# Performance work log

Hardware: AMD Instinct MI355X
Metric: run time of the kernel (lower is better)

Reference implementation:

```python
import jax, jax.numpy as jnp
import numpy as np

L = 16384   # nodes (rows)
E = 131072  # edges
SP = 20000  # column positions (nodes + periodic images)
C = 512     # embed_dim
H = 8       # heads
DH = C // H # head dim = 64
HID = 1024  # ffn hidden


def setup_inputs() -> dict:
    key = jax.random.key(0)
    ks = jax.random.split(key, 16)
    p = lambda k, shape: jax.random.normal(k, shape, dtype=jnp.float32) * 0.02
    return dict(
        x=jax.random.normal(ks[0], (L, C), dtype=jnp.float32),
        row_index=jax.random.randint(ks[1], (E,), 0, L),
        col_index=jax.random.randint(ks[2], (E,), 0, L),
        to_col_index=jax.random.randint(ks[3], (E,), 0, SP),
        att_bias=jax.random.normal(ks[4], (E, H), dtype=jnp.float32),
        pos_att_bias=jax.random.normal(ks[5], (E, H), dtype=jnp.float32),
        dist=jax.random.uniform(ks[6], (E,), minval=0.5, maxval=5.0),
        pos=jax.random.normal(ks[7], (L, 3), dtype=jnp.float32),
        col_pos=jax.random.normal(ks[8], (SP, 3), dtype=jnp.float32),
        ln1_g=jnp.ones((C,), jnp.float32), ln1_b=jnp.zeros((C,), jnp.float32),
        ln2_g=jnp.ones((C,), jnp.float32), ln2_b=jnp.zeros((C,), jnp.float32),
        Wq=p(ks[9], (C, C)), bq=jnp.zeros((C,), jnp.float32),
        Wk=p(ks[10], (C, C)), bk=jnp.zeros((C,), jnp.float32),
        Wv=p(ks[11], (C, C)), bv=jnp.zeros((C,), jnp.float32),
        Wvec=p(ks[12], (3, C)), bvec=jnp.zeros((C,), jnp.float32),
        Wo=p(ks[13], (C, C)), bo=jnp.zeros((C,), jnp.float32),
        W1=p(ks[14], (C, HID)), b1=jnp.zeros((HID,), jnp.float32),
        W2=p(ks[15], (HID, C)), b2=jnp.zeros((C,), jnp.float32),
    )


def _ln(x, g, b, eps=1e-5):
    mu = jnp.mean(x, -1, keepdims=True)
    v = jnp.mean((x - mu) ** 2, -1, keepdims=True)
    return (x - mu) * jax.lax.rsqrt(v + eps) * g + b


def reference(x, row_index, col_index, to_col_index, att_bias, pos_att_bias,
              dist, pos, col_pos, ln1_g, ln1_b, ln2_g, ln2_b,
              Wq, bq, Wk, bk, Wv, bv, Wvec, bvec, Wo, bo, W1, b1, W2, b2):
    Lx = x.shape[0]
    # --- pre-norm + Euclidean sparse attention ---
    z = _ln(x, ln1_g, ln1_b)
    q = (z @ Wq + bq).reshape(Lx, H, DH)
    k = (z @ Wk + bk).reshape(Lx, H, DH)
    v = (z @ Wv + bv).reshape(Lx, H, DH)
    qe = q[row_index]          # (E,H,DH) gather
    ke = k[col_index]          # (E,H,DH)
    ve = v[col_index]          # (E,H,DH)
    # relative unit direction from receiving node to (PBC-shifted) column node
    rel = (col_pos[to_col_index] - pos[row_index]) / dist[:, None]   # (E,3)
    ve = ve + (rel @ Wvec + bvec).reshape(-1, H, DH)
    # Euclidean (negative squared L2) attention score + positional bias
    score = -jnp.sum((qe - ke) ** 2, axis=-1) / np.float32(np.sqrt(DH)) + pos_att_bias  # (E,H)
    # segment softmax over edges grouped by row_index
    m = jax.ops.segment_max(score, row_index, num_segments=Lx)       # (L,H)
    m = jnp.where(jnp.isfinite(m), m, 0.0)
    pexp = jnp.exp(score - m[row_index])
    den = jax.ops.segment_sum(pexp, row_index, num_segments=Lx)      # (L,H)
    deng = den[row_index]
    alpha = pexp / jnp.where(deng == 0.0, 1.0, deng)                 # (E,H)
    out = jax.ops.segment_sum(alpha[:, :, None] * ve, row_index, num_segments=Lx)
    att = out.reshape(Lx, C) @ Wo + bo
    x = x + att
    # --- pre-norm + feed-forward ---
    z2 = _ln(x, ln2_g, ln2_b)
    ff = jax.nn.gelu(z2 @ W1 + b1) @ W2 + b2
    return x + ff
```

## Files before the change

### kernel.cpp

```cpp
#include <hip/hip_runtime.h>

#define L_NODES 16384
#define E_EDGES 131072
#define CDIM 512
#define QKVDIM 1536
#define HEADS 8
#define DHEAD 64
#define HID 1024

typedef __attribute__((ext_vector_type(8))) short bf16x8;
typedef __attribute__((ext_vector_type(4))) float f32x4;

__device__ inline unsigned short f2b(float f) {
    union { float f; unsigned int u; } v{f};
    unsigned int r = (v.u + 0x7fffu + ((v.u >> 16) & 1u)) >> 16;
    return (unsigned short)r;
}
__device__ inline float b2f(unsigned short h) {
    union { unsigned int u; float f; } v;
    v.u = (unsigned int)h << 16;
    return v.f;
}

__device__ inline void async_lds16(const void* g, void* l) {
    __builtin_amdgcn_global_load_lds(
        (const __attribute__((address_space(1))) unsigned int*)g,
        (__attribute__((address_space(3))) unsigned int*)l,
        16, 0, 0);
}

__global__ __launch_bounds__(256) void ln_bf16_kernel(
    const float* __restrict__ x, const float* __restrict__ g,
    const float* __restrict__ b, short* __restrict__ out)
{
    int row = blockIdx.x;
    int t = threadIdx.x;
    const float2* xr = (const float2*)(x + (size_t)row * CDIM);
    float2 v = xr[t];
    float s = v.x + v.y;
    float sq = v.x * v.x + v.y * v.y;
    for (int off = 32; off; off >>= 1) {
        s += __shfl_xor(s, off);
        sq += __shfl_xor(sq, off);
    }
    __shared__ float ss[4], sqs[4];
    int wave = t >> 6, lane = t & 63;
    if (lane == 0) { ss[wave] = s; sqs[wave] = sq; }
    __syncthreads();
    s = ss[0] + ss[1] + ss[2] + ss[3];
    sq = sqs[0] + sqs[1] + sqs[2] + sqs[3];
    float mu = s * (1.0f / CDIM);
    float var = sq * (1.0f / CDIM) - mu * mu;
    float inv = rsqrtf(var + 1e-5f);
    int c = t * 2;
    unsigned short h0 = f2b((v.x - mu) * inv * g[c] + b[c]);
    unsigned short h1 = f2b((v.y - mu) * inv * g[c + 1] + b[c + 1]);
    unsigned int packed = ((unsigned int)h1 << 16) | h0;
    *(unsigned int*)(out + (size_t)row * CDIM + c) = packed;
}

__global__ __launch_bounds__(256) void prep_kernel(
    const float* __restrict__ Wq, const float* __restrict__ Wk,
    const float* __restrict__ Wv, const float* __restrict__ Wo,
    const float* __restrict__ W1, const float* __restrict__ W2,
    short* __restrict__ wqkvT, short* __restrict__ woT,
    short* __restrict__ w1T, short* __restrict__ w2T,
    const float* __restrict__ bq, const float* __restrict__ bk,
    const float* __restrict__ bv, float* __restrict__ bqkv,
    int* __restrict__ cnt)
{
    int bid = blockIdx.x;
    if (bid >= 2054) {
        cnt[(bid - 2054) * 256 + threadIdx.x] = 0;
        return;
    }
    if (bid >= 2048) {
        int i = (bid - 2048) * 256 + threadIdx.x;
        float val = (i < CDIM) ? bq[i] : (i < 2 * CDIM) ? bk[i - CDIM] : bv[i - 2 * CDIM];
        bqkv[i] = val;
        return;
    }
    const float* W; short* WT; int K, N, tn, tk;
    if (bid < 1024) {
        int w = bid >> 8, local = bid & 255;
        tn = local & 15; tk = local >> 4; K = 512; N = 512;
        W = (w == 0) ? Wq : (w == 1) ? Wk : (w == 2) ? Wv : Wo;
        WT = (w == 3) ? woT : wqkvT + (size_t)w * 512 * 512;
    } else if (bid < 1536) {
        int local = bid - 1024;
        tn = local & 31; tk = local >> 5; K = 512; N = 1024;
        W = W1; WT = w1T;
    } else {
        int local = bid - 1536;
        tn = local & 15; tk = local >> 4; K = 1024; N = 512;
        W = W2; WT = w2T;
    }
    __shared__ float tile[32][33];
    int tx = threadIdx.x & 31, ty = threadIdx.x >> 5;
    int n0 = tn * 32, k0 = tk * 32;
#pragma unroll
    for (int r = 0; r < 4; r++)
        tile[ty + r * 8][tx] = W[(size_t)(k0 + ty + r * 8) * N + n0 + tx];
    __syncthreads();
#pragma unroll
    for (int r = 0; r < 4; r++)
        WT[(size_t)(n0 + ty + r * 8) * K + k0 + tx] = f2b(tile[tx][ty + r * 8]);
}

template<int BM>
__global__ __launch_bounds__(256) void gemm_bf16_kernel(
    const short* __restrict__ A, const short* __restrict__ B,
    const float* __restrict__ bias, const float* __restrict__ res,
    float* __restrict__ outf, short* __restrict__ outb,
    int M, int N, int K, int act)
{
    constexpr int MI = BM / 32;
    constexpr int LPI_A = BM / 64;
    constexpr int STAGE_A = BM * 64;
    constexpr int STAGE_B = 8192;
    __shared__ short As[3 * BM * 32];
    __shared__ short Bs[3 * 128 * 32];
    int t = threadIdx.x;
    int bm = blockIdx.y * BM, bn = blockIdx.x * 128;
    int wave = t >> 6, lane = t & 63;
    int wm = (wave & 1) * (BM / 2), wn = (wave >> 1) * 64;
    int crow = lane & 15, quad = lane >> 4;

    f32x4 acc[MI][4] = {};

    const int niter = K >> 5;
    auto stage = [&](int s, int k0) {
#pragma unroll
        for (int a = 0; a < LPI_A; a++) {
            int idx = a * 256 + t;
            int row = idx >> 2, chunk = idx & 3;
            async_lds16(A + (size_t)(bm + row) * K + k0 + chunk * 8,
                        (char*)As + s * STAGE_A + idx * 16);
        }
#pragma unroll
        for (int c = 0; c < 2; c++) {
            int idx = c * 256 + t;
            int row = idx >> 2, chunk = idx & 3;
            async_lds16(B + (size_t)(bn + row) * K + k0 + chunk * 8,
                        (char*)Bs + s * STAGE_B + idx * 16);
        }
    };

    stage(0, 0);
    stage(1, 32);

    for (int i = 0; i < niter; ++i) {
        int cur = i % 3;
        if (i + 1 < niter) {
            if constexpr (BM == 128) asm volatile("s_waitcnt vmcnt(4)" ::: "memory");
            else                     asm volatile("s_waitcnt vmcnt(3)" ::: "memory");
        } else {
            asm volatile("s_waitcnt vmcnt(0)" ::: "memory");
        }
        __builtin_amdgcn_s_barrier();
        if (i + 2 < niter) stage((i + 2) % 3, (i + 2) << 5);

        const short* Ab = As + cur * (BM * 32);
        const short* Bb = Bs + cur * (128 * 32);
        bf16x8 af[MI], bg[4];
#pragma unroll
        for (int ii = 0; ii < MI; ii++)
            af[ii] = *(const bf16x8*)&Ab[(wm + ii * 16 + crow) * 32 + quad * 8];
#pragma unroll
        for (int j = 0; j < 4; j++)
            bg[j] = *(const bf16x8*)&Bb[(wn + j * 16 + crow) * 32 + quad * 8];
#pragma unroll
        for (int ii = 0; ii < MI; ii++)
#pragma unroll
            for (int j = 0; j < 4; j++)
                acc[ii][j] = __builtin_amdgcn_mfma_f32_16x16x32_bf16(af[ii], bg[j], acc[ii][j], 0, 0, 0);
    }

#pragma unroll
    for (int i = 0; i < MI; i++) {
#pragma unroll
        for (int j = 0; j < 4; j++) {
            int n = bn + wn + j * 16 + crow;
            float bi = bias ? bias[n] : 0.0f;
#pragma unroll
            for (int r = 0; r < 4; r++) {
                int mrow = bm + wm + i * 16 + quad * 4 + r;
                float val = acc[i][j][r] + bi;
                if (act) {
                    float u = 1.5957691216057308f * (val + 0.044715f * val * val * val);
                    val = val / (1.0f + __expf(-u));
                }
                if (res) val += res[(size_t)mrow * N + n];
                if (outf) outf[(size_t)mrow * N + n] = val;
                if (outb) outb[(size_t)mrow * N + n] = f2b(val);
            }
        }
    }
}

__global__ void hist_kernel(const int* __restrict__ row_index, int* __restrict__ cnt)
{
    int e = blockIdx.x * 256 + threadIdx.x;
    if (e < E_EDGES) atomicAdd(&cnt[row_index[e]], 1);
}

__global__ void scan_kernel(const int* __restrict__ cnt, int* __restrict__ row_start,
                            int* __restrict__ cursor)
{
    int t = threadIdx.x;
    const int PER = L_NODES / 64;
    int local = 0;
    for (int i = 0; i < PER; i++) local += cnt[t * PER + i];
    int v = local;
    for (int off = 1; off < 64; off <<= 1) {
        int u = __shfl_up(v, off);
        if (t >= off) v += u;
    }
    int run = v - local;
    for (int i = 0; i < PER; i++) {
        row_start[t * PER + i] = run;
        cursor[t * PER + i] = run;
        run += cnt[t * PER + i];
    }
    if (t == 63) row_start[L_NODES] = run;
}

__global__ void scatter_kernel(const int* __restrict__ row_index, const int* __restrict__ col_index,
                               const int* __restrict__ to_col_index, const float* __restrict__ dist,
                               const float* __restrict__ pos, const float* __restrict__ col_pos,
                               const float* __restrict__ pos_att_bias,
                               int* __restrict__ cursor, int4* __restrict__ emeta,
                               float* __restrict__ pabp)
{
    int e = blockIdx.x * 256 + threadIdx.x;
    if (e < E_EDGES) {
        int row = row_index[e];
        int p = atomicAdd(&cursor[row], 1);
        int tci = to_col_index[e];
        float dinv = 1.0f / dist[e];
        float r0 = (col_pos[tci * 3]     - pos[row * 3])     * dinv;
        float r1 = (col_pos[tci * 3 + 1] - pos[row * 3 + 1]) * dinv;
        float r2 = (col_pos[tci * 3 + 2] - pos[row * 3 + 2]) * dinv;
        emeta[p] = make_int4(col_index[e], __float_as_int(r0), __float_as_int(r1),
                             __float_as_int(r2));
        const float4* pb = (const float4*)(pos_att_bias + (size_t)e * HEADS);
        float4 b0 = pb[0], b1 = pb[1];
        float4* dst = (float4*)(pabp + (size_t)p * HEADS);
        dst[0] = b0; dst[1] = b1;
    }
}

__global__ __launch_bounds__(256) void attn_kernel(
    const short* __restrict__ qkv, const int4* __restrict__ emeta,
    const float* __restrict__ pabp, const int* __restrict__ row_start,
    const float* __restrict__ Wvec, const float* __restrict__ bvec,
    short* __restrict__ out_bf)
{
    int lane = threadIdx.x & 63;
    int r = blockIdx.x * 4 + (threadIdx.x >> 6);
    int h = lane >> 3;
    int cbase = lane * 8;

    float qv[8], wv0[8], wv1[8], wv2[8], bvv[8];
    {
        bf16x8 qh = *(const bf16x8*)(qkv + (size_t)r * QKVDIM + cbase);
#pragma unroll
        for (int j = 0; j < 8; j++) qv[j] = b2f((unsigned short)qh[j]);
        float4 a0 = *(const float4*)(Wvec + cbase);
        float4 a1 = *(const float4*)(Wvec + cbase + 4);
        float4 b0 = *(const float4*)(Wvec + CDIM + cbase);
        float4 b1 = *(const float4*)(Wvec + CDIM + cbase + 4);
        float4 c0 = *(const float4*)(Wvec + 2 * CDIM + cbase);
        float4 c1 = *(const float4*)(Wvec + 2 * CDIM + cbase + 4);
        float4 d0 = *(const float4*)(bvec + cbase);
        float4 d1 = *(const float4*)(bvec + cbase + 4);
        wv0[0]=a0.x; wv0[1]=a0.y; wv0[2]=a0.z; wv0[3]=a0.w; wv0[4]=a1.x; wv0[5]=a1.y; wv0[6]=a1.z; wv0[7]=a1.w;
        wv1[0]=b0.x; wv1[1]=b0.y; wv1[2]=b0.z; wv1[3]=b0.w; wv1[4]=b1.x; wv1[5]=b1.y; wv1[6]=b1.z; wv1[7]=b1.w;
        wv2[0]=c0.x; wv2[1]=c0.y; wv2[2]=c0.z; wv2[3]=c0.w; wv2[4]=c1.x; wv2[5]=c1.y; wv2[6]=c1.z; wv2[7]=c1.w;
        bvv[0]=d0.x; bvv[1]=d0.y; bvv[2]=d0.z; bvv[3]=d0.w; bvv[4]=d1.x; bvv[5]=d1.y; bvv[6]=d1.z; bvv[7]=d1.w;
    }

    int e0 = row_start[r], e1 = row_start[r + 1];
    float m = -1e30f, l = 0.0f;
    float acc[8] = {};

    int4 em_n, em_n2;
    float pab_n;
    bf16x8 k_n, v_n;
    if (e0 < e1) {
        em_n = emeta[e0];
        em_n2 = emeta[(e0 + 1 < e1) ? e0 + 1 : e1 - 1];
        pab_n = pabp[(size_t)e0 * HEADS + h];
        const short* kp = qkv + (size_t)em_n.x * QKVDIM + CDIM + cbase;
        k_n = *(const bf16x8*)kp;
        v_n = *(const bf16x8*)(kp + CDIM);
    }
    for (int idx = e0; idx < e1; ++idx) {
        int4 em = em_n;
        float pab = pab_n;
        bf16x8 k8 = k_n, v8 = v_n;
        em_n = em_n2;
        int i2 = (idx + 2 < e1) ? idx + 2 : e1 - 1;
        em_n2 = emeta[i2];
        int i1 = (idx + 1 < e1) ? idx + 1 : e1 - 1;
        pab_n = pabp[(size_t)i1 * HEADS + h];
        {
            const short* kp = qkv + (size_t)em_n.x * QKVDIM + CDIM + cbase;
            k_n = *(const bf16x8*)kp;
            v_n = *(const bf16x8*)(kp + CDIM);
        }
        float s = 0.0f;
        float vf[8];
#pragma unroll
        for (int j = 0; j < 8; j++) {
            float kf = b2f((unsigned short)k8[j]);
            vf[j] = b2f((unsigned short)v8[j]);
            float d = qv[j] - kf;
            s = fmaf(d, d, s);
        }
        s += __shfl_xor(s, 1);
        s += __shfl_xor(s, 2);
        s += __shfl_xor(s, 4);
        float score = -s * 0.125f + pab;
        float mn = fmaxf(m, score);
        float scale = __expf(m - mn);
        float pexp = __expf(score - mn);
        m = mn;
        l = l * scale + pexp;
        float r0 = __int_as_float(em.y), r1 = __int_as_float(em.z), r2 = __int_as_float(em.w);
#pragma unroll
        for (int j = 0; j < 8; j++) {
            float vv = vf[j] + r0 * wv0[j] + r1 * wv1[j] + r2 * wv2[j] + bvv[j];
            acc[j] = fmaf(acc[j], scale, pexp * vv);
        }
    }
    float inv = (l > 0.0f) ? 1.0f / l : 0.0f;
    bf16x8 o;
#pragma unroll
    for (int j = 0; j < 8; j++) o[j] = (short)f2b(acc[j] * inv);
    *(bf16x8*)(out_bf + (size_t)r * CDIM + cbase) = o;
}

extern "C" void kernel_launch(void* const* d_in, const int* in_sizes, int n_in,
                              void* d_out, int out_size, void* d_ws, size_t ws_size,
                              hipStream_t stream)
{
    const float* x            = (const float*)d_in[0];
    const int*   row_index    = (const int*)d_in[1];
    const int*   col_index    = (const int*)d_in[2];
    const int*   to_col_index = (const int*)d_in[3];
    const float* pos_att_bias = (const float*)d_in[5];
    const float* dist         = (const float*)d_in[6];
    const float* pos          = (const float*)d_in[7];
    const float* col_pos      = (const float*)d_in[8];
    const float* ln1_g = (const float*)d_in[9];
    const float* ln1_b = (const float*)d_in[10];
    const float* ln2_g = (const float*)d_in[11];
    const float* ln2_b = (const float*)d_in[12];
    const float* Wq = (const float*)d_in[13];  const float* bq = (const float*)d_in[14];
    const float* Wk = (const float*)d_in[15];  const float* bk = (const float*)d_in[16];
    const float* Wv = (const float*)d_in[17];  const float* bv = (const float*)d_in[18];
    const float* Wvec = (const float*)d_in[19]; const float* bvec = (const float*)d_in[20];
    const float* Wo = (const float*)d_in[21];  const float* bo = (const float*)d_in[22];
    const float* W1 = (const float*)d_in[23];  const float* b1 = (const float*)d_in[24];
    const float* W2 = (const float*)d_in[25];  const float* b2 = (const float*)d_in[26];

    char* ws = (char*)d_ws;
    size_t off = 0;
    auto alloc = [&](size_t bytes) -> void* {
        void* p = ws + off;
        off = (off + bytes + 255) & ~(size_t)255;
        return p;
    };
    const size_t LC = (size_t)L_NODES * CDIM;
    short* qkvb = (short*)alloc((size_t)L_NODES * QKVDIM * 2);
    float* x1f  = (float*)alloc(LC * 4);
    short* zbf  = (short*)alloc(LC * 2);
    short* abf  = (short*)alloc(LC * 2);
    short* wqkvT = (short*)alloc((size_t)QKVDIM * CDIM * 2);
    short* woT   = (short*)alloc((size_t)CDIM * CDIM * 2);
    short* w1T   = (short*)alloc((size_t)CDIM * HID * 2);
    short* w2T   = (short*)alloc((size_t)HID * CDIM * 2);
    float* bqkv  = (float*)alloc(QKVDIM * 4);
    int* cnt       = (int*)alloc(L_NODES * 4);
    int* cursor    = (int*)alloc(L_NODES * 4);
    int* row_start = (int*)alloc((L_NODES + 1) * 4);
    int4* emeta    = (int4*)alloc((size_t)E_EDGES * 16);
    short* hbf = (short*)qkvb;
    float* pabp = x1f;

    prep_kernel<<<2118, 256, 0, stream>>>(Wq, Wk, Wv, Wo, W1, W2,
                                          wqkvT, woT, w1T, w2T,
                                          bq, bk, bv, bqkv, cnt);

    ln_bf16_kernel<<<L_NODES, 256, 0, stream>>>(x, ln1_g, ln1_b, zbf);

    dim3 gqkv(QKVDIM / 128, L_NODES / 128);
    gemm_bf16_kernel<128><<<gqkv, 256, 0, stream>>>(zbf, wqkvT, bqkv, nullptr, nullptr, qkvb,
                                                    L_NODES, QKVDIM, CDIM, 0);

    hist_kernel<<<E_EDGES / 256, 256, 0, stream>>>(row_index, cnt);
    scan_kernel<<<1, 64, 0, stream>>>(cnt, row_start, cursor);
    scatter_kernel<<<E_EDGES / 256, 256, 0, stream>>>(row_index, col_index, to_col_index,
                                                      dist, pos, col_pos, pos_att_bias,
                                                      cursor, emeta, pabp);

    attn_kernel<<<L_NODES / 4, 256, 0, stream>>>(qkvb, emeta, pabp, row_start, Wvec, bvec, abf);

    dim3 gwo(CDIM / 128, L_NODES / 64);
    gemm_bf16_kernel<64><<<gwo, 256, 0, stream>>>(abf, woT, bo, x, x1f, nullptr, L_NODES, CDIM, CDIM, 0);

    ln_bf16_kernel<<<L_NODES, 256, 0, stream>>>(x1f, ln2_g, ln2_b, zbf);

    dim3 g1024(HID / 128, L_NODES / 128);
    gemm_bf16_kernel<128><<<g1024, 256, 0, stream>>>(zbf, w1T, b1, nullptr, nullptr, hbf, L_NODES, HID, CDIM, 1);
    dim3 gw2(CDIM / 128, L_NODES / 64);
    gemm_bf16_kernel<64><<<gw2, 256, 0, stream>>>(hbf, w2T, b2, x1f, (float*)d_out, nullptr, L_NODES, CDIM, HID, 0);
}
```

Measured before the change: 411.6 us.

## Load GEMM operands directly from global into registers, dropping LDS staging

Replaces the triple-buffered async global-to-LDS pipeline in the bf16 GEMM with per-wave direct global loads into registers, software-prefetching the next K-slice into a second register set. This removes LDS traffic, barriers and waitcnt bookkeeping. In exchange, operand tiles shared across waves are no longer reused through LDS, so each wave refetches A and B from global/L2. The access pattern is also narrower, with 16-byte strided row loads.

```diff
diff --git a/kernel.cpp b/kernel.cpp
--- a/kernel.cpp
+++ b/kernel.cpp
@@ -20,13 +20,6 @@
     union { unsigned int u; float f; } v;
     v.u = (unsigned int)h << 16;
     return v.f;
-}
-
-__device__ inline void async_lds16(const void* g, void* l) {
-    __builtin_amdgcn_global_load_lds(
-        (const __attribute__((address_space(1))) unsigned int*)g,
-        (__attribute__((address_space(3))) unsigned int*)l,
-        16, 0, 0);
 }
 
 __global__ __launch_bounds__(256) void ln_bf16_kernel(
@@ -115,11 +108,6 @@
     int M, int N, int K, int act)
 {
     constexpr int MI = BM / 32;
-    constexpr int LPI_A = BM / 64;
-    constexpr int STAGE_A = BM * 64;
-    constexpr int STAGE_B = 8192;
-    __shared__ short As[3 * BM * 32];
-    __shared__ short Bs[3 * 128 * 32];
     int t = threadIdx.x;
     int bm = blockIdx.y * BM, bn = blockIdx.x * 128;
     int wave = t >> 6, lane = t & 63;
@@ -128,52 +116,40 @@
 
     f32x4 acc[MI][4] = {};
 
+    const short* Ap[MI];
+    const short* Bp[4];
+#pragma unroll
+    for (int i = 0; i < MI; i++)
+        Ap[i] = A + (size_t)(bm + wm + i * 16 + crow) * K + quad * 8;
+#pragma unroll
+    for (int j = 0; j < 4; j++)
+        Bp[j] = B + (size_t)(bn + wn + j * 16 + crow) * K + quad * 8;
+
+    bf16x8 a_n[MI], b_n[4];
+#pragma unroll
+    for (int i = 0; i < MI; i++) a_n[i] = *(const bf16x8*)Ap[i];
+#pragma unroll
+    for (int j = 0; j < 4; j++)  b_n[j] = *(const bf16x8*)Bp[j];
+
     const int niter = K >> 5;
-    auto stage = [&](int s, int k0) {
-#pragma unroll
-        for (int a = 0; a < LPI_A; a++) {
-            int idx = a * 256 + t;
-            int row = idx >> 2, chunk = idx & 3;
-            async_lds16(A + (size_t)(bm + row) * K + k0 + chunk * 8,
-                        (char*)As + s * STAGE_A + idx * 16);
-        }
-#pragma unroll
-        for (int c = 0; c < 2; c++) {
-            int idx = c * 256 + t;
-            int row = idx >> 2, chunk = idx & 3;
-            async_lds16(B + (size_t)(bn + row) * K + k0 + chunk * 8,
-                        (char*)Bs + s * STAGE_B + idx * 16);
-        }
-    };
-
-    stage(0, 0);
-    stage(1, 32);
-
-    for (int i = 0; i < niter; ++i) {
-        int cur = i % 3;
-        if (i + 1 < niter) {
-            if constexpr (BM == 128) asm volatile("s_waitcnt vmcnt(4)" ::: "memory");
-            else                     asm volatile("s_waitcnt vmcnt(3)" ::: "memory");
-        } else {
-            asm volatile("s_waitcnt vmcnt(0)" ::: "memory");
-        }
-        __builtin_amdgcn_s_barrier();
-        if (i + 2 < niter) stage((i + 2) % 3, (i + 2) << 5);
-
-        const short* Ab = As + cur * (BM * 32);
-        const short* Bb = Bs + cur * (128 * 32);
-        bf16x8 af[MI], bg[4];
-#pragma unroll
-        for (int ii = 0; ii < MI; ii++)
-            af[ii] = *(const bf16x8*)&Ab[(wm + ii * 16 + crow) * 32 + quad * 8];
-#pragma unroll
-        for (int j = 0; j < 4; j++)
-            bg[j] = *(const bf16x8*)&Bb[(wn + j * 16 + crow) * 32 + quad * 8];
-#pragma unroll
-        for (int ii = 0; ii < MI; ii++)
+    for (int it = 0; it < niter; ++it) {
+        bf16x8 a_c[MI], b_c[4];
+#pragma unroll
+        for (int i = 0; i < MI; i++) a_c[i] = a_n[i];
+#pragma unroll
+        for (int j = 0; j < 4; j++)  b_c[j] = b_n[j];
+        if (it + 1 < niter) {
+            int off = (it + 1) << 5;
+#pragma unroll
+            for (int i = 0; i < MI; i++) a_n[i] = *(const bf16x8*)(Ap[i] + off);
+#pragma unroll
+            for (int j = 0; j < 4; j++)  b_n[j] = *(const bf16x8*)(Bp[j] + off);
+        }
+#pragma unroll
+        for (int i = 0; i < MI; i++)
 #pragma unroll
             for (int j = 0; j < 4; j++)
-                acc[ii][j] = __builtin_amdgcn_mfma_f32_16x16x32_bf16(af[ii], bg[j], acc[ii][j], 0, 0, 0);
+                acc[i][j] = __builtin_amdgcn_mfma_f32_16x16x32_bf16(a_c[i], b_c[j], acc[i][j], 0, 0, 0);
     }
 
 #pragma unroll
```

Result: slower. 568.0 us (+38.0%).
